# Optimization experiments

Hardware: AMD Instinct MI355X
Metric: run time of the kernel (lower is better)

The kernel has to match this reference:

```python
import jax, jax.numpy as jnp
import numpy as np

H, P = 16, 4  # n_heads, n_points


def setup_inputs() -> dict:
    B, L, D = 2, 4096, 1024
    rng = jax.random.key(0)
    ks = jax.random.split(rng, 12)
    w = lambda k, shape, s=0.02: jax.random.normal(k, shape, jnp.float32) * s
    return {
        "query": jax.random.normal(ks[0], (B, L, D), jnp.float32),
        "key": jax.random.normal(ks[1], (B, L, D), jnp.float32),
        "value": jax.random.normal(ks[2], (B, L, D), jnp.float32),
        "w_qk": w(ks[3], (D, 2 * D)), "b_qk": jnp.zeros((2 * D,), jnp.float32),
        "w_value": w(ks[4], (D, D)), "b_value": jnp.zeros((D,), jnp.float32),
        "w_off": w(ks[5], (D, H * P * 2)), "b_off": w(ks[6], (H * P * 2,), 0.3),
        "w_attw": w(ks[7], (D, H * P)), "b_attw": jnp.zeros((H * P,), jnp.float32),
        "w_out": w(ks[8], (D, D)), "b_out": jnp.zeros((D,), jnp.float32),
    }


def reference(query, key, value, w_qk, b_qk, w_value, b_value, w_off, b_off,
              w_attw, b_attw, w_out, b_out):
    B, L, D = value.shape
    Dh = D // H
    _qk = query @ w_qk + b_qk  # computed in torch forward but unused (dead code)
    # value projection -> (B, H, L, Dh)
    v = (value @ w_value + b_value).reshape(B, L, H, Dh).transpose(0, 2, 1, 3)
    off = (query @ w_off + b_off).reshape(B, L, H, P, 2)
    attw = jax.nn.softmax((query @ w_attw + b_attw).reshape(B, L, H, P), axis=-1)
    # effective reference point for query l (after the [:, :, :, :1, :] slice): (x=0, y=l/(L-1))
    ref_y = jnp.linspace(0.0, 1.0, L)
    sx = jnp.clip(off[..., 0], 0.0, 1.0)                                   # (B,L,H,P)
    sy = jnp.clip(ref_y[None, :, None, None] + off[..., 1], 0.0, 1.0)
    # F.grid_sample, align_corners=False, padding zeros, input shape (B*H, Dh, 1, L)
    ix = ((sx + 1.0) * L - 1.0) * 0.5
    iy = ((sy + 1.0) * 1.0 - 1.0) * 0.5
    x0 = jnp.floor(ix)
    fx = ix - x0
    x0i = x0.astype(jnp.int32)
    x1i = x0i + 1
    m0 = ((x0i >= 0) & (x0i < L)).astype(v.dtype)
    m1 = ((x1i >= 0) & (x1i < L)).astype(v.dtype)
    y0 = jnp.floor(iy)
    fy = iy - y0
    # height dim is 1: only row 0 valid, zero padding otherwise
    hy = jnp.where(y0 == 0.0, 1.0 - fy, 0.0) + jnp.where(y0 == -1.0, fy, 0.0)
    tr = lambda a: a.transpose(0, 2, 1, 3)  # (B,L,H,P) -> (B,H,L,P)

    def gather(idx):  # idx: (B,H,L,P) int32
        idxc = jnp.clip(idx, 0, L - 1).reshape(B, H, L * P, 1)
        return jnp.take_along_axis(v, idxc, axis=2).reshape(B, H, L, P, Dh)

    val0 = gather(tr(x0i))
    val1 = gather(tr(x1i))
    wx0 = tr((1.0 - fx) * m0 * hy)
    wx1 = tr(fx * m1 * hy)
    sampled = val0 * wx0[..., None] + val1 * wx1[..., None]  # (B,H,L,P,Dh)
    out = jnp.einsum('bhlpd,bhlp->blhd', sampled, tr(attw)).reshape(B, L, D)
    return out @ w_out + b_out
```

## Files before the change

kernel.cpp:

```cpp
#include <hip/hip_runtime.h>
#include <hip/hip_bf16.h>

typedef __bf16 bf16x8 __attribute__((ext_vector_type(8)));
typedef float f32x4 __attribute__((ext_vector_type(4)));

static __device__ __forceinline__ unsigned short f2bf(float x) {
    __hip_bfloat16 b = __float2bfloat16(x);
    return __builtin_bit_cast(unsigned short, b);
}
static __device__ __forceinline__ float bf2f(unsigned short u) {
    __hip_bfloat16 b = __builtin_bit_cast(__hip_bfloat16, u);
    return __bfloat162float(b);
}

static __device__ __forceinline__ void gload_lds16(const void* g, void* l) {
    __builtin_amdgcn_global_load_lds(
        (const __attribute__((address_space(1))) void*)g,
        (__attribute__((address_space(3))) void*)l, 16, 0, 0);
}

__global__ __launch_bounds__(256) void prep_all(
    const float* __restrict__ w_value, const float* __restrict__ w_out,
    const float* __restrict__ w_off, const float* __restrict__ w_attw,
    const float* __restrict__ value,
    unsigned short* __restrict__ WvT, unsigned short* __restrict__ WoT,
    unsigned short* __restrict__ WThi, unsigned short* __restrict__ WTlo,
    unsigned short* __restrict__ Vbf) {
    const int bid = blockIdx.x;
    const int tid = threadIdx.x;
    if (bid >= 2240) {
        int g = (bid - 2240) * 256 + tid;
        int r4 = g >> 8;
        int cpos = g & 255;
        int b = r4 / 2176;
        int l = 1920 + (r4 % 2176);
        size_t off4 = (size_t)(b * 4096 + l) * 256 + cpos;
        float4 v = reinterpret_cast<const float4*>(value)[off4];
        ushort4 o;
        o.x = f2bf(v.x); o.y = f2bf(v.y); o.z = f2bf(v.z); o.w = f2bf(v.w);
        reinterpret_cast<ushort4*>(Vbf)[off4] = o;
        return;
    }
    __shared__ float tile[32][33];
    const int sel = bid >> 5;
    const int k0 = (bid & 31) * 32;
    const int tx = tid & 31, ty = tid >> 5;
    if (sel < 64) {
        const float* in = (sel < 32) ? w_value : w_out;
        unsigned short* out = (sel < 32) ? WvT : WoT;
        const int n0 = (sel & 31) * 32;
        for (int i = ty; i < 32; i += 8) tile[i][tx] = in[(size_t)(k0 + i) * 1024 + n0 + tx];
        __syncthreads();
        for (int i = ty; i < 32; i += 8)
            out[(size_t)(n0 + i) * 1024 + k0 + tx] = f2bf(tile[tx][i]);
    } else {
        const int n0 = (sel - 64) * 32;
        for (int i = ty; i < 32; i += 8) {
            int n = n0 + tx;
            tile[i][tx] = (n < 128) ? w_off[(size_t)(k0 + i) * 128 + n]
                                    : w_attw[(size_t)(k0 + i) * 64 + (n - 128)];
        }
        __syncthreads();
        for (int i = ty; i < 32; i += 8) {
            int n = n0 + i, k = k0 + tx;
            float v = tile[tx][i];
            unsigned short hi = f2bf(v);
            unsigned short lo = f2bf(v - bf2f(hi));
            WThi[(size_t)n * 1024 + k] = hi;
            WTlo[(size_t)n * 1024 + k] = lo;
        }
    }
}

__global__ __launch_bounds__(256, 2) void fused_mfma(
    const float* __restrict__ query,
    const unsigned short* __restrict__ WThi,
    const unsigned short* __restrict__ WTlo,
    float* __restrict__ part,
    const unsigned short* __restrict__ Vbf,
    const unsigned short* __restrict__ WvT,
    const float* __restrict__ b_value,
    unsigned short* __restrict__ Vproj) {
    __shared__ unsigned short smem[16384];
    const int bid = blockIdx.x;
    const int tid = threadIdx.x;
    const int lane = tid & 63, wave = tid >> 6;
    const int r = lane & 15, kq = lane >> 4;

    if (bid < 512) {
        unsigned short* Ahi = smem;
        unsigned short* Alo = smem + 2048;
        unsigned short* Bs2 = smem + 4096;
        const int bm = (bid & 127) * 64;
        const int sk = bid >> 7;

        f32x4 acc[4][3];
        #pragma unroll
        for (int i = 0; i < 4; ++i)
            #pragma unroll
            for (int j = 0; j < 3; ++j) acc[i][j] = (f32x4){0.f, 0.f, 0.f, 0.f};

        const int arow = tid >> 2;
        const int apos = (tid & 3) * 8;

        for (int k0 = sk * 256; k0 < sk * 256 + 256; k0 += 32) {
            const float* qp = query + (size_t)(bm + arow) * 1024 + k0 + apos;
            float4 qa = reinterpret_cast<const float4*>(qp)[0];
            float4 qb = reinterpret_cast<const float4*>(qp)[1];
            unsigned int hw[4], lw[4];
            {
                float4 qf[2] = {qa, qb};
                #pragma unroll
                for (int t = 0; t < 2; ++t) {
                    float e0 = qf[t].x, e1 = qf[t].y, e2 = qf[t].z, e3 = qf[t].w;
                    unsigned short h0 = f2bf(e0), h1 = f2bf(e1), h2 = f2bf(e2), h3 = f2bf(e3);
                    unsigned short l0 = f2bf(e0 - bf2f(h0)), l1 = f2bf(e1 - bf2f(h1));
                    unsigned short l2 = f2bf(e2 - bf2f(h2)), l3 = f2bf(e3 - bf2f(h3));
                    hw[t * 2] = (unsigned int)h0 | ((unsigned int)h1 << 16);
                    hw[t * 2 + 1] = (unsigned int)h2 | ((unsigned int)h3 << 16);
                    lw[t * 2] = (unsigned int)l0 | ((unsigned int)l1 << 16);
                    lw[t * 2 + 1] = (unsigned int)l2 | ((unsigned int)l3 << 16);
                }
            }
            *reinterpret_cast<uint4*>(&Ahi[arow * 32 + apos]) = (uint4){hw[0], hw[1], hw[2], hw[3]};
            *reinterpret_cast<uint4*>(&Alo[arow * 32 + apos]) = (uint4){lw[0], lw[1], lw[2], lw[3]};
            #pragma unroll
            for (int t = 0; t < 6; ++t) {
                int c = tid + 256 * t;
                int plane = (c >= 768);
                int cp = c - 768 * plane;
                const unsigned short* src = (plane ? WTlo : WThi)
                    + (size_t)(cp >> 2) * 1024 + k0 + (cp & 3) * 8;
                gload_lds16(src, &Bs2[(size_t)(c & ~63) * 8]);
            }
            __syncthreads();

            bf16x8 bh[3], bl[3];
            #pragma unroll
            for (int j = 0; j < 3; ++j) {
                int ro = (wave * 48 + j * 16 + r) * 32 + kq * 8;
                bh[j] = *reinterpret_cast<const bf16x8*>(&Bs2[ro]);
                bl[j] = *reinterpret_cast<const bf16x8*>(&Bs2[192 * 32 + ro]);
            }
            #pragma unroll
            for (int i = 0; i < 4; ++i) {
                int ro = (i * 16 + r) * 32 + kq * 8;
                bf16x8 ah = *reinterpret_cast<const bf16x8*>(&Ahi[ro]);
                bf16x8 al = *reinterpret_cast<const bf16x8*>(&Alo[ro]);
                #pragma unroll
                for (int j = 0; j < 3; ++j) {
                    acc[i][j] = __builtin_amdgcn_mfma_f32_16x16x32_bf16(ah, bh[j], acc[i][j], 0, 0, 0);
                    acc[i][j] = __builtin_amdgcn_mfma_f32_16x16x32_bf16(ah, bl[j], acc[i][j], 0, 0, 0);
                    acc[i][j] = __builtin_amdgcn_mfma_f32_16x16x32_bf16(al, bh[j], acc[i][j], 0, 0, 0);
                }
            }
            __syncthreads();
        }

        float* P = part + (size_t)sk * 8192 * 192;
        #pragma unroll
        for (int i = 0; i < 4; ++i) {
            int row0 = bm + i * 16 + kq * 4;
            #pragma unroll
            for (int j = 0; j < 3; ++j) {
                int col = wave * 48 + j * 16 + r;
                #pragma unroll
                for (int rr = 0; rr < 4; ++rr)
                    P[(size_t)(row0 + rr) * 192 + col] = acc[i][j][rr];
            }
        }
    } else {
        unsigned short* As = smem;
        unsigned short* Bs = smem + 4096;
        const int b2 = bid - 512;
        const int bx = b2 % 17;
        const int by = (b2 / 17) & 15;
        const int bz = b2 / 272;
        const int bm = 1920 + bz * 4096 + bx * 128;
        const int bn = by * 64;

        f32x4 acc[2][4];
        #pragma unroll
        for (int i = 0; i < 2; ++i)
            #pragma unroll
            for (int j = 0; j < 4; ++j) acc[i][j] = (f32x4){0.f, 0.f, 0.f, 0.f};

        const int c1 = tid;
        const int c2 = 256 + tid;

        for (int k0 = 0; k0 < 1024; k0 += 32) {
            gload_lds16(Vbf + (size_t)(bm + (c1 >> 2)) * 1024 + k0 + (c1 & 3) * 8,
                        &As[(size_t)(c1 & ~63) * 8]);
            gload_lds16(Vbf + (size_t)(bm + (c2 >> 2)) * 1024 + k0 + (c2 & 3) * 8,
                        &As[(size_t)(256 + (tid & ~63)) * 8]);
            gload_lds16(WvT + (size_t)(bn + (tid >> 2)) * 1024 + k0 + (tid & 3) * 8,
                        &Bs[(size_t)(tid & ~63) * 8]);
            __syncthreads();

            bf16x8 af[2], bfr[4];
            #pragma unroll
            for (int i = 0; i < 2; ++i)
                af[i] = *reinterpret_cast<const bf16x8*>(&As[(wave * 32 + i * 16 + r) * 32 + kq * 8]);
            #pragma unroll
            for (int j = 0; j < 4; ++j)
                bfr[j] = *reinterpret_cast<const bf16x8*>(&Bs[(j * 16 + r) * 32 + kq * 8]);
            #pragma unroll
            for (int i = 0; i < 2; ++i)
                #pragma unroll
                for (int j = 0; j < 4; ++j)
                    acc[i][j] = __builtin_amdgcn_mfma_f32_16x16x32_bf16(af[i], bfr[j], acc[i][j], 0, 0, 0);
            __syncthreads();
        }

        #pragma unroll
        for (int i = 0; i < 2; ++i) {
            int row0 = bm + wave * 32 + i * 16 + kq * 4;
            #pragma unroll
            for (int j = 0; j < 4; ++j) {
                int col = bn + j * 16 + r;
                float bs = b_value[col];
                #pragma unroll
                for (int rr = 0; rr < 4; ++rr)
                    Vproj[(size_t)(row0 + rr) * 1024 + col] = f2bf(acc[i][j][rr] + bs);
            }
        }
    }
}

__global__ __launch_bounds__(256) void sample_coef(
    const float* __restrict__ part, const float* __restrict__ b_off,
    const float* __restrict__ b_attw, const unsigned short* __restrict__ vproj,
    unsigned short* __restrict__ s_out) {
    const int n = blockIdx.x;
    const int tid = threadIdx.x;
    const int l = n & 4095;
    __shared__ float Ls[192];
    __shared__ int sIdx[64];
    __shared__ float sC0[64], sC1[64];
    if (tid < 192) {
        const size_t SK = (size_t)8192 * 192;
        const float* Pn = part + (size_t)n * 192 + tid;
        float s = (tid < 128) ? b_off[tid] : b_attw[tid - 128];
        Ls[tid] = s + Pn[0] + Pn[SK] + Pn[2 * SK] + Pn[3 * SK];
    }
    __syncthreads();
    if (tid < 64) {
        int h = tid >> 2, p = tid & 3;
        float l0 = Ls[128 + h * 4 + 0], l1 = Ls[128 + h * 4 + 1];
        float l2 = Ls[128 + h * 4 + 2], l3 = Ls[128 + h * 4 + 3];
        float mx = fmaxf(fmaxf(l0, l1), fmaxf(l2, l3));
        float e0 = expf(l0 - mx), e1 = expf(l1 - mx), e2 = expf(l2 - mx), e3 = expf(l3 - mx);
        float esum = e0 + e1 + e2 + e3;
        float aw = ((p == 0) ? e0 : (p == 1) ? e1 : (p == 2) ? e2 : e3) / esum;
        float o0 = Ls[h * 8 + p * 2], o1 = Ls[h * 8 + p * 2 + 1];
        float sx = fminf(fmaxf(o0, 0.f), 1.f);
        float ry = (float)l / 4095.0f;
        float sy = fminf(fmaxf(ry + o1, 0.f), 1.f);
        float ix = ((sx + 1.f) * 4096.f - 1.f) * 0.5f;
        float iy = sy * 0.5f;
        float x0f = floorf(ix);
        float fx = ix - x0f;
        int x0 = (int)x0f;
        int x1 = x0 + 1;
        float m0 = (x0 >= 0 && x0 < 4096) ? 1.f : 0.f;
        float m1 = (x1 >= 0 && x1 < 4096) ? 1.f : 0.f;
        float y0f = floorf(iy);
        float fy = iy - y0f;
        float hy = ((y0f == 0.f) ? (1.f - fy) : 0.f) + ((y0f == -1.f) ? fy : 0.f);
        sC0[tid] = aw * (1.f - fx) * m0 * hy;
        sC1[tid] = aw * fx * m1 * hy;
        sIdx[tid] = x0 < 0 ? 0 : (x0 > 4095 ? 4095 : x0);
    }
    __syncthreads();
    const int d = tid * 4;
    const int h = tid >> 4;
    const size_t vb = (size_t)(n >> 12) * 4096 * 1024;
    float a0 = 0.f, a1 = 0.f, a2 = 0.f, a3 = 0.f;
    #pragma unroll
    for (int p = 0; p < 4; ++p) {
        int e = h * 4 + p;
        int x0 = sIdx[e];
        float c0 = sC0[e], c1 = sC1[e];
        int x1 = (x0 + 1 > 4095) ? 4095 : x0 + 1;
        ushort4 v0 = *reinterpret_cast<const ushort4*>(vproj + vb + (size_t)x0 * 1024 + d);
        ushort4 v1 = *reinterpret_cast<const ushort4*>(vproj + vb + (size_t)x1 * 1024 + d);
        a0 += c0 * bf2f(v0.x) + c1 * bf2f(v1.x);
        a1 += c0 * bf2f(v0.y) + c1 * bf2f(v1.y);
        a2 += c0 * bf2f(v0.z) + c1 * bf2f(v1.z);
        a3 += c0 * bf2f(v0.w) + c1 * bf2f(v1.w);
    }
    ushort4 o;
    o.x = f2bf(a0); o.y = f2bf(a1); o.z = f2bf(a2); o.w = f2bf(a3);
    *reinterpret_cast<ushort4*>(s_out + (size_t)n * 1024 + d) = o;
}

__global__ __launch_bounds__(256, 2) void gemm_bt(
    const unsigned short* __restrict__ A,
    const unsigned short* __restrict__ Bt,
    const float* __restrict__ bias,
    float* __restrict__ C, int N, int K) {
    __shared__ unsigned short As[128 * 32];
    __shared__ unsigned short Bs[128 * 32];
    const int tid = threadIdx.x;
    const int lane = tid & 63;
    const int wave = tid >> 6;
    const int bm = blockIdx.x * 128;
    const int bn = blockIdx.y * 128;
    const int wr = wave >> 1;
    const int wc = wave & 1;
    const int r = lane & 15;
    const int kq = lane >> 4;

    f32x4 acc[4][4];
    #pragma unroll
    for (int i = 0; i < 4; ++i)
        #pragma unroll
        for (int j = 0; j < 4; ++j) acc[i][j] = (f32x4){0.f, 0.f, 0.f, 0.f};

    const int c1 = tid;
    const int c2 = 256 + tid;
    const int cb1 = wave * 64;
    const int cb2 = 256 + wave * 64;

    for (int k0 = 0; k0 < K; k0 += 32) {
        const unsigned short* Ab = A + (size_t)bm * K + k0;
        const unsigned short* Bb = Bt + (size_t)bn * K + k0;
        gload_lds16(Ab + (size_t)(c1 >> 2) * K + (c1 & 3) * 8, &As[cb1 * 8]);
        gload_lds16(Ab + (size_t)(c2 >> 2) * K + (c2 & 3) * 8, &As[cb2 * 8]);
        gload_lds16(Bb + (size_t)(c1 >> 2) * K + (c1 & 3) * 8, &Bs[cb1 * 8]);
        gload_lds16(Bb + (size_t)(c2 >> 2) * K + (c2 & 3) * 8, &Bs[cb2 * 8]);
        __syncthreads();

        bf16x8 af[4], bfr[4];
        #pragma unroll
        for (int i = 0; i < 4; ++i)
            af[i] = *reinterpret_cast<const bf16x8*>(&As[(wr * 64 + i * 16 + r) * 32 + kq * 8]);
        #pragma unroll
        for (int j = 0; j < 4; ++j)
            bfr[j] = *reinterpret_cast<const bf16x8*>(&Bs[(wc * 64 + j * 16 + r) * 32 + kq * 8]);
        #pragma unroll
        for (int i = 0; i < 4; ++i)
            #pragma unroll
            for (int j = 0; j < 4; ++j)
                acc[i][j] = __builtin_amdgcn_mfma_f32_16x16x32_bf16(af[i], bfr[j], acc[i][j], 0, 0, 0);
        __syncthreads();
    }

    #pragma unroll
    for (int i = 0; i < 4; ++i) {
        int row0 = bm + wr * 64 + i * 16 + kq * 4;
        #pragma unroll
        for (int j = 0; j < 4; ++j) {
            int col = bn + wc * 64 + j * 16 + r;
            float bs = bias[col];
            #pragma unroll
            for (int rr = 0; rr < 4; ++rr)
                C[(size_t)(row0 + rr) * N + col] = acc[i][j][rr] + bs;
        }
    }
}

extern "C" void kernel_launch(void* const* d_in, const int* in_sizes, int n_in,
                              void* d_out, int out_size, void* d_ws, size_t ws_size,
                              hipStream_t stream) {
    const float* query  = (const float*)d_in[0];
    const float* value  = (const float*)d_in[2];
    const float* w_value = (const float*)d_in[5];
    const float* b_value = (const float*)d_in[6];
    const float* w_off   = (const float*)d_in[7];
    const float* b_off   = (const float*)d_in[8];
    const float* w_attw  = (const float*)d_in[9];
    const float* b_attw  = (const float*)d_in[10];
    const float* w_out   = (const float*)d_in[11];
    const float* b_out   = (const float*)d_in[12];
    float* out = (float*)d_out;

    char* w = (char*)d_ws;
    unsigned short* Vbf   = (unsigned short*)(w);
    unsigned short* WvT   = (unsigned short*)(w + (16ull << 20));
    unsigned short* WoT   = (unsigned short*)(w + (18ull << 20));
    unsigned short* Vproj = (unsigned short*)(w + (20ull << 20));
    unsigned short* S     = (unsigned short*)(w + (36ull << 20));
    unsigned short* WThi  = (unsigned short*)(w + (53ull << 20));
    unsigned short* WTlo  = (unsigned short*)(w + (54ull << 20));
    float*          Part  = (float*)(w + (56ull << 20));

    prep_all<<<6592, 256, 0, stream>>>(w_value, w_out, w_off, w_attw, value,
                                       WvT, WoT, WThi, WTlo, Vbf);
    fused_mfma<<<1056, 256, 0, stream>>>(query, WThi, WTlo, Part, Vbf, WvT, b_value, Vproj);
    sample_coef<<<8192, 256, 0, stream>>>(Part, b_off, b_attw, Vproj, S);
    gemm_bt<<<dim3(64, 8), 256, 0, stream>>>(S, WoT, b_out, out, 1024, 1024);
}
```

Before: 94.46 us.

## Drop split-K in logits GEMM and enlarge value-projection tiles with swizzle

```diff
diff --git a/kernel.cpp b/kernel.cpp
--- a/kernel.cpp
+++ b/kernel.cpp
@@ -76,54 +76,44 @@
     const float* __restrict__ query,
     const unsigned short* __restrict__ WThi,
     const unsigned short* __restrict__ WTlo,
-    float* __restrict__ part,
+    float* __restrict__ logits,
     const unsigned short* __restrict__ Vbf,
     const unsigned short* __restrict__ WvT,
     const float* __restrict__ b_value,
     unsigned short* __restrict__ Vproj) {
-    __shared__ unsigned short smem[16384];
+    __shared__ unsigned short smem[14336];
     const int bid = blockIdx.x;
     const int tid = threadIdx.x;
     const int lane = tid & 63, wave = tid >> 6;
     const int r = lane & 15, kq = lane >> 4;
 
-    if (bid < 512) {
+    if (bid < 256) {
         unsigned short* Ahi = smem;
-        unsigned short* Alo = smem + 2048;
-        unsigned short* Bs2 = smem + 4096;
-        const int bm = (bid & 127) * 64;
-        const int sk = bid >> 7;
-
-        f32x4 acc[4][3];
-        #pragma unroll
-        for (int i = 0; i < 4; ++i)
+        unsigned short* Alo = smem + 1280;
+        unsigned short* Bs2 = smem + 2560;
+        const int bm = bid * 32;
+
+        f32x4 acc[2][3];
+        #pragma unroll
+        for (int i = 0; i < 2; ++i)
             #pragma unroll
             for (int j = 0; j < 3; ++j) acc[i][j] = (f32x4){0.f, 0.f, 0.f, 0.f};
 
-        const int arow = tid >> 2;
-        const int apos = (tid & 3) * 8;
-
-        for (int k0 = sk * 256; k0 < sk * 256 + 256; k0 += 32) {
+        const int arow = tid >> 3;
+        const int apos = (tid & 7) * 4;
+
+        for (int k0 = 0; k0 < 1024; k0 += 32) {
             const float* qp = query + (size_t)(bm + arow) * 1024 + k0 + apos;
-            float4 qa = reinterpret_cast<const float4*>(qp)[0];
-            float4 qb = reinterpret_cast<const float4*>(qp)[1];
-            unsigned int hw[4], lw[4];
-            {
-                float4 qf[2] = {qa, qb};
-                #pragma unroll
-                for (int t = 0; t < 2; ++t) {
-                    float e0 = qf[t].x, e1 = qf[t].y, e2 = qf[t].z, e3 = qf[t].w;
-                    unsigned short h0 = f2bf(e0), h1 = f2bf(e1), h2 = f2bf(e2), h3 = f2bf(e3);
-                    unsigned short l0 = f2bf(e0 - bf2f(h0)), l1 = f2bf(e1 - bf2f(h1));
-                    unsigned short l2 = f2bf(e2 - bf2f(h2)), l3 = f2bf(e3 - bf2f(h3));
-                    hw[t * 2] = (unsigned int)h0 | ((unsigned int)h1 << 16);
-                    hw[t * 2 + 1] = (unsigned int)h2 | ((unsigned int)h3 << 16);
-                    lw[t * 2] = (unsigned int)l0 | ((unsigned int)l1 << 16);
-                    lw[t * 2 + 1] = (unsigned int)l2 | ((unsigned int)l3 << 16);
-                }
-            }
-            *reinterpret_cast<uint4*>(&Ahi[arow * 32 + apos]) = (uint4){hw[0], hw[1], hw[2], hw[3]};
-            *reinterpret_cast<uint4*>(&Alo[arow * 32 + apos]) = (uint4){lw[0], lw[1], lw[2], lw[3]};
+            float4 qa = *reinterpret_cast<const float4*>(qp);
+            unsigned short h0 = f2bf(qa.x), h1 = f2bf(qa.y), h2 = f2bf(qa.z), h3 = f2bf(qa.w);
+            unsigned short l0 = f2bf(qa.x - bf2f(h0)), l1 = f2bf(qa.y - bf2f(h1));
+            unsigned short l2 = f2bf(qa.z - bf2f(h2)), l3 = f2bf(qa.w - bf2f(h3));
+            uint2 hv = {(unsigned int)h0 | ((unsigned int)h1 << 16),
+                        (unsigned int)h2 | ((unsigned int)h3 << 16)};
+            uint2 lv = {(unsigned int)l0 | ((unsigned int)l1 << 16),
+                        (unsigned int)l2 | ((unsigned int)l3 << 16)};
+            *reinterpret_cast<uint2*>(&Ahi[arow * 40 + apos]) = hv;
+            *reinterpret_cast<uint2*>(&Alo[arow * 40 + apos]) = lv;
             #pragma unroll
             for (int t = 0; t < 6; ++t) {
                 int c = tid + 256 * t;
@@ -143,8 +133,8 @@
                 bl[j] = *reinterpret_cast<const bf16x8*>(&Bs2[192 * 32 + ro]);
             }
             #pragma unroll
-            for (int i = 0; i < 4; ++i) {
-                int ro = (i * 16 + r) * 32 + kq * 8;
+            for (int i = 0; i < 2; ++i) {
+                int ro = (i * 16 + r) * 40 + kq * 8;
                 bf16x8 ah = *reinterpret_cast<const bf16x8*>(&Ahi[ro]);
                 bf16x8 al = *reinterpret_cast<const bf16x8*>(&Alo[ro]);
                 #pragma unroll
@@ -157,55 +147,59 @@
             __syncthreads();
         }
 
-        float* P = part + (size_t)sk * 8192 * 192;
-        #pragma unroll
-        for (int i = 0; i < 4; ++i) {
+        #pragma unroll
+        for (int i = 0; i < 2; ++i) {
             int row0 = bm + i * 16 + kq * 4;
             #pragma unroll
             for (int j = 0; j < 3; ++j) {
                 int col = wave * 48 + j * 16 + r;
                 #pragma unroll
                 for (int rr = 0; rr < 4; ++rr)
-                    P[(size_t)(row0 + rr) * 192 + col] = acc[i][j][rr];
+                    logits[(size_t)(row0 + rr) * 192 + col] = acc[i][j][rr];
             }
         }
     } else {
         unsigned short* As = smem;
         unsigned short* Bs = smem + 4096;
-        const int b2 = bid - 512;
-        const int bx = b2 % 17;
-        const int by = (b2 / 17) & 15;
-        const int bz = b2 / 272;
+        const int vb = bid - 256;
+        const int swz = (vb & 7) * 34 + (vb >> 3);
+        const int bz = (swz >= 136) ? 1 : 0;
+        const int wk = swz - 136 * bz;
+        const int bx = wk >> 3;
+        const int by = wk & 7;
         const int bm = 1920 + bz * 4096 + bx * 128;
-        const int bn = by * 64;
-
-        f32x4 acc[2][4];
-        #pragma unroll
-        for (int i = 0; i < 2; ++i)
+        const int bn = by * 128;
+        const int wr = wave >> 1, wc = wave & 1;
+
+        f32x4 acc[4][4];
+        #pragma unroll
+        for (int i = 0; i < 4; ++i)
             #pragma unroll
             for (int j = 0; j < 4; ++j) acc[i][j] = (f32x4){0.f, 0.f, 0.f, 0.f};
 
         const int c1 = tid;
         const int c2 = 256 + tid;
+        const int cb1 = wave * 64;
+        const int cb2 = 256 + wave * 64;
 
         for (int k0 = 0; k0 < 1024; k0 += 32) {
-            gload_lds16(Vbf + (size_t)(bm + (c1 >> 2)) * 1024 + k0 + (c1 & 3) * 8,
-                        &As[(size_t)(c1 & ~63) * 8]);
-            gload_lds16(Vbf + (size_t)(bm + (c2 >> 2)) * 1024 + k0 + (c2 & 3) * 8,
-                        &As[(size_t)(256 + (tid & ~63)) * 8]);
-            gload_lds16(WvT + (size_t)(bn + (tid >> 2)) * 1024 + k0 + (tid & 3) * 8,
-                        &Bs[(size_t)(tid & ~63) * 8]);
+            const unsigned short* Ab = Vbf + (size_t)bm * 1024 + k0;
+            const unsigned short* Bb = WvT + (size_t)bn * 1024 + k0;
+            gload_lds16(Ab + (size_t)(c1 >> 2) * 1024 + (c1 & 3) * 8, &As[cb1 * 8]);
+            gload_lds16(Ab + (size_t)(c2 >> 2) * 1024 + (c2 & 3) * 8, &As[cb2 * 8]);
+            gload_lds16(Bb + (size_t)(c1 >> 2) * 1024 + (c1 & 3) * 8, &Bs[cb1 * 8]);
+            gload_lds16(Bb + (size_t)(c2 >> 2) * 1024 + (c2 & 3) * 8, &Bs[cb2 * 8]);
             __syncthreads();
 
-            bf16x8 af[2], bfr[4];
-            #pragma unroll
-            for (int i = 0; i < 2; ++i)
-                af[i] = *reinterpret_cast<const bf16x8*>(&As[(wave * 32 + i * 16 + r) * 32 + kq * 8]);
+            bf16x8 af[4], bfr[4];
+            #pragma unroll
+            for (int i = 0; i < 4; ++i)
+                af[i] = *reinterpret_cast<const bf16x8*>(&As[(wr * 64 + i * 16 + r) * 32 + kq * 8]);
             #pragma unroll
             for (int j = 0; j < 4; ++j)
-                bfr[j] = *reinterpret_cast<const bf16x8*>(&Bs[(j * 16 + r) * 32 + kq * 8]);
-            #pragma unroll
-            for (int i = 0; i < 2; ++i)
+                bfr[j] = *reinterpret_cast<const bf16x8*>(&Bs[(wc * 64 + j * 16 + r) * 32 + kq * 8]);
+            #pragma unroll
+            for (int i = 0; i < 4; ++i)
                 #pragma unroll
                 for (int j = 0; j < 4; ++j)
                     acc[i][j] = __builtin_amdgcn_mfma_f32_16x16x32_bf16(af[i], bfr[j], acc[i][j], 0, 0, 0);
@@ -213,11 +207,11 @@
         }
 
         #pragma unroll
-        for (int i = 0; i < 2; ++i) {
-            int row0 = bm + wave * 32 + i * 16 + kq * 4;
+        for (int i = 0; i < 4; ++i) {
+            int row0 = bm + wr * 64 + i * 16 + kq * 4;
             #pragma unroll
             for (int j = 0; j < 4; ++j) {
-                int col = bn + j * 16 + r;
+                int col = bn + wc * 64 + j * 16 + r;
                 float bs = b_value[col];
                 #pragma unroll
                 for (int rr = 0; rr < 4; ++rr)
@@ -228,7 +222,7 @@
 }
 
 __global__ __launch_bounds__(256) void sample_coef(
-    const float* __restrict__ part, const float* __restrict__ b_off,
+    const float* __restrict__ logits, const float* __restrict__ b_off,
     const float* __restrict__ b_attw, const unsigned short* __restrict__ vproj,
     unsigned short* __restrict__ s_out) {
     const int n = blockIdx.x;
@@ -238,10 +232,8 @@
     __shared__ int sIdx[64];
     __shared__ float sC0[64], sC1[64];
     if (tid < 192) {
-        const size_t SK = (size_t)8192 * 192;
-        const float* Pn = part + (size_t)n * 192 + tid;
         float s = (tid < 128) ? b_off[tid] : b_attw[tid - 128];
-        Ls[tid] = s + Pn[0] + Pn[SK] + Pn[2 * SK] + Pn[3 * SK];
+        Ls[tid] = s + logits[(size_t)n * 192 + tid];
     }
     __syncthreads();
     if (tid < 64) {
@@ -383,11 +375,11 @@
     unsigned short* S     = (unsigned short*)(w + (36ull << 20));
     unsigned short* WThi  = (unsigned short*)(w + (53ull << 20));
     unsigned short* WTlo  = (unsigned short*)(w + (54ull << 20));
-    float*          Part  = (float*)(w + (56ull << 20));
+    float*          Logits= (float*)(w + (56ull << 20));
 
     prep_all<<<6592, 256, 0, stream>>>(w_value, w_out, w_off, w_attw, value,
                                        WvT, WoT, WThi, WTlo, Vbf);
-    fused_mfma<<<1056, 256, 0, stream>>>(query, WThi, WTlo, Part, Vbf, WvT, b_value, Vproj);
-    sample_coef<<<8192, 256, 0, stream>>>(Part, b_off, b_attw, Vproj, S);
+    fused_mfma<<<528, 256, 0, stream>>>(query, WThi, WTlo, Logits, Vbf, WvT, b_value, Vproj);
+    sample_coef<<<8192, 256, 0, stream>>>(Logits, b_off, b_attw, Vproj, S);
     gemm_bt<<<dim3(64, 8), 256, 0, stream>>>(S, WoT, b_out, out, 1024, 1024);
 }
```

Result: slower. 97.07 us (+2.8%).
